# Kernel optimization log

Measured on AMD Instinct MI355X. Metric: run time of the kernel, lower is better.

## Reference

```python
import jax, jax.numpy as jnp
import numpy as np

NUM_HEADS = 16
KEY_SIZE = 128
D_MODEL = NUM_HEADS * KEY_SIZE  # 2048; model_size defaults to num_heads*key_size
B, S = 4, 4096
EPS = 1e-6
MASK_NEG = -1e9


def setup_inputs() -> dict:
    key = jax.random.key(0)
    ks = jax.random.split(key, 8)
    query = jax.random.normal(ks[0], (B, S, D_MODEL), dtype=jnp.float32)
    key_t = jax.random.normal(ks[1], (B, S, D_MODEL), dtype=jnp.float32)
    value = jax.random.normal(ks[2], (B, S, D_MODEL), dtype=jnp.float32)
    # mask broadcast-added to attn_logits of shape [B, S, H, H]; 1 = masked out
    mask = jax.random.randint(ks[3], (B, S, NUM_HEADS, NUM_HEADS), 0, 2).astype(jnp.float32)
    w_scale = 0.02
    Wq = jax.random.normal(ks[4], (D_MODEL, NUM_HEADS * KEY_SIZE), dtype=jnp.float32) * w_scale
    Wk = jax.random.normal(ks[5], (D_MODEL, NUM_HEADS * KEY_SIZE), dtype=jnp.float32) * w_scale
    Wv = jax.random.normal(ks[6], (D_MODEL, NUM_HEADS * KEY_SIZE), dtype=jnp.float32) * w_scale
    Wo = jax.random.normal(ks[7], (NUM_HEADS * KEY_SIZE, D_MODEL), dtype=jnp.float32) * w_scale
    return {"query": query, "key": key_t, "value": value, "mask": mask,
            "Wq": Wq, "Wk": Wk, "Wv": Wv, "Wo": Wo}


def _split_heads(x):
    # [B, S, H*D] -> [B, H, S, D]  (matches tf reshape + transpose(0,2,1,3))
    b, s, _ = x.shape
    return x.reshape(b, s, NUM_HEADS, KEY_SIZE).transpose(0, 2, 1, 3)


def reference(query, key, value, mask, Wq, Wk, Wv, Wo):
    qh = _split_heads(query @ Wq)   # [B, H, S, D]
    kh = _split_heads(key @ Wk)     # [B, H, S, D]
    vh = _split_heads(value @ Wv)   # [B, H, S, D]

    # sum_normalization=True
    qh = qh / (jnp.sum(qh, axis=-1, keepdims=True) + EPS)
    kh = kh / (jnp.sum(kh, axis=-1, keepdims=True) + EPS)

    # Literal tf einsum '...thd,...Thd->...htT' on [B,H,S,D] tensors:
    # t/T bind to the head axis, h binds to the sequence axis.
    # attn_logits: [B, S, H, H]
    attn_logits = jnp.einsum('bqsd,bksd->bsqk', qh, kh)
    attn_logits = attn_logits + mask * MASK_NEG

    # use_softmax=True
    attn_weights = jax.nn.softmax(attn_logits / np.sqrt(float(KEY_SIZE)), axis=-1)

    # Literal tf einsum '...htT,...Thd->...thd' -> [B, H, S, D]
    attn = jnp.einsum('bsqk,bksd->bqsd', attn_weights, vh)
    # _combine_heads: transpose(0,2,1,3) then reshape -> [B, S, H*D]
    attn = attn.transpose(0, 2, 1, 3).reshape(attn.shape[0], attn.shape[2], NUM_HEADS * KEY_SIZE)
    out = attn @ Wo
    return (out, attn_weights)
```

## Files before the change

### kernel.cpp

```cpp
#include <hip/hip_runtime.h>
#include <hip/hip_fp16.h>

#define NHEAD 16
#define DHEAD 128
#define DMODEL 2048
#define SEQ 4096
#define BATCH 4
#define MROWS (BATCH*SEQ)

typedef _Float16 f16x8 __attribute__((ext_vector_type(8)));
typedef _Float16 f16x4 __attribute__((ext_vector_type(4)));
typedef float f32x4 __attribute__((ext_vector_type(4)));

__device__ inline void split8(const float* __restrict__ x, _Float16* __restrict__ hi,
                              _Float16* __restrict__ lo, int i8) {
  float4 v0 = ((const float4*)x)[2 * i8];
  float4 v1 = ((const float4*)x)[2 * i8 + 1];
  f16x8 h, l;
  h[0] = (_Float16)v0.x; h[1] = (_Float16)v0.y;
  h[2] = (_Float16)v0.z; h[3] = (_Float16)v0.w;
  h[4] = (_Float16)v1.x; h[5] = (_Float16)v1.y;
  h[6] = (_Float16)v1.z; h[7] = (_Float16)v1.w;
  ((f16x8*)hi)[i8] = h;
  if (lo) {
    l[0] = (_Float16)(v0.x - (float)h[0]);
    l[1] = (_Float16)(v0.y - (float)h[1]);
    l[2] = (_Float16)(v0.z - (float)h[2]);
    l[3] = (_Float16)(v0.w - (float)h[3]);
    l[4] = (_Float16)(v1.x - (float)h[4]);
    l[5] = (_Float16)(v1.y - (float)h[5]);
    l[6] = (_Float16)(v1.z - (float)h[6]);
    l[7] = (_Float16)(v1.w - (float)h[7]);
    ((f16x8*)lo)[i8] = l;
  }
}

__global__ __launch_bounds__(256) void split_f32_f16(
    const float* __restrict__ x, _Float16* __restrict__ hi,
    _Float16* __restrict__ lo, int n8) {
  int i = blockIdx.x * blockDim.x + threadIdx.x;
  int stride = gridDim.x * blockDim.x;
  for (; i < n8; i += stride) split8(x, hi, lo, i);
}

__device__ inline void transpose_body(const float* __restrict__ W,
                                      _Float16* __restrict__ hi,
                                      _Float16* __restrict__ lo,
                                      int bx, int by, int tx, int ty) {
  __shared__ float tile[32][33];
  int c = bx * 32 + tx;
  for (int r0 = 0; r0 < 32; r0 += 8) {
    int r = by * 32 + ty + r0;
    tile[ty + r0][tx] = W[(size_t)r * DMODEL + c];
  }
  __syncthreads();
  for (int r0 = 0; r0 < 32; r0 += 8) {
    int n = bx * 32 + ty + r0;
    int k = by * 32 + tx;
    float v = tile[tx][ty + r0];
    _Float16 h = (_Float16)v;
    hi[(size_t)n * DMODEL + k] = h;
    if (lo) lo[(size_t)n * DMODEL + k] = (_Float16)(v - (float)h);
  }
}

__global__ __launch_bounds__(256) void transpose_split(
    const float* __restrict__ W, _Float16* __restrict__ hi,
    _Float16* __restrict__ lo) {
  transpose_body(W, hi, lo, blockIdx.x, blockIdx.y, threadIdx.x, threadIdx.y);
}

__device__ inline void colsum_body(const float* __restrict__ W,
                                   float* __restrict__ CS, int k, int t) {
  const int h = t >> 4, s = t & 15;
  double acc = 0.0;
  const float* p = W + (size_t)k * DMODEL + h * DHEAD + s * 8;
#pragma unroll
  for (int i = 0; i < 8; i++) acc += (double)p[i];
#pragma unroll
  for (int m = 1; m < 16; m <<= 1) acc += __shfl_xor(acc, m, 64);
  if (s == 0) CS[(size_t)h * DMODEL + k] = (float)acc;
}

__global__ __launch_bounds__(256) void colsum_f64(
    const float* __restrict__ W, float* __restrict__ CS) {
  colsum_body(W, CS, blockIdx.x, threadIdx.x);
}

__global__ __launch_bounds__(256) void weights_prep(
    const float* __restrict__ Wq, const float* __restrict__ Wk,
    const float* __restrict__ Wv, const float* __restrict__ Wo,
    _Float16* __restrict__ qh, _Float16* __restrict__ ql,
    _Float16* __restrict__ kh, _Float16* __restrict__ kl,
    _Float16* __restrict__ vh, _Float16* __restrict__ oh,
    float* __restrict__ CSq, float* __restrict__ CSk) {
  const int z = blockIdx.z;
  const int t = threadIdx.y * 32 + threadIdx.x;
  if (z == 4) {
    int id = blockIdx.y * 64 + blockIdx.x;
    const float* W = (id & 2048) ? Wk : Wq;
    float* CS = (id & 2048) ? CSk : CSq;
    colsum_body(W, CS, id & 2047, t);
    return;
  }
  const float* W; _Float16* hi; _Float16* lo;
  switch (z) {
    case 0:  W = Wq; hi = qh; lo = ql;      break;
    case 1:  W = Wk; hi = kh; lo = kl;      break;
    case 2:  W = Wv; hi = vh; lo = nullptr; break;
    default: W = Wo; hi = oh; lo = nullptr; break;
  }
  transpose_body(W, hi, lo, blockIdx.x, blockIdx.y, threadIdx.x, threadIdx.y);
}

__global__ __launch_bounds__(256) void prep_qkv(
    const float* __restrict__ q, const float* __restrict__ k,
    const float* __restrict__ v,
    const float* __restrict__ CSq, const float* __restrict__ CSk,
    _Float16* __restrict__ qh, _Float16* __restrict__ ql,
    _Float16* __restrict__ kh, _Float16* __restrict__ kl,
    _Float16* __restrict__ vh,
    float* __restrict__ rsQ, float* __restrict__ rsK) {
  const float* X; const float* CS; float* rs;
  _Float16* hi; _Float16* lo;
  if (blockIdx.y == 0)      { X = q; CS = CSq; rs = rsQ; hi = qh; lo = ql; }
  else if (blockIdx.y == 1) { X = k; CS = CSk; rs = rsK; hi = kh; lo = kl; }
  else                      { X = v; CS = nullptr; rs = nullptr; hi = vh; lo = nullptr; }
  const int t = threadIdx.x;
  const int lane = t & 63, w = t >> 6;
  const int row0 = blockIdx.x * 8 + w * 2;

  const float4* x0 = (const float4*)(X + ((size_t)row0 << 11));
  const float4* x1 = (const float4*)(X + ((size_t)(row0 + 1) << 11));
  float4 xa[8], xb[8];
#pragma unroll
  for (int i = 0; i < 8; i++) {
    xa[i] = x0[i * 64 + lane];
    xb[i] = x1[i * 64 + lane];
  }

  f16x4* hi4 = (f16x4*)hi;
  f16x4* lo4 = (f16x4*)lo;
  const size_t rb0 = (size_t)row0 << 9;
  const size_t rb1 = (size_t)(row0 + 1) << 9;
#pragma unroll
  for (int i = 0; i < 8; i++) {
    int c = i * 64 + lane;
    float4 a = xa[i], b = xb[i];
    f16x4 ha, hb;
    ha[0] = (_Float16)a.x; ha[1] = (_Float16)a.y;
    ha[2] = (_Float16)a.z; ha[3] = (_Float16)a.w;
    hb[0] = (_Float16)b.x; hb[1] = (_Float16)b.y;
    hb[2] = (_Float16)b.z; hb[3] = (_Float16)b.w;
    hi4[rb0 + c] = ha;
    hi4[rb1 + c] = hb;
    if (lo) {
      f16x4 la, lb;
      la[0] = (_Float16)(a.x - (float)ha[0]);
      la[1] = (_Float16)(a.y - (float)ha[1]);
      la[2] = (_Float16)(a.z - (float)ha[2]);
      la[3] = (_Float16)(a.w - (float)ha[3]);
      lb[0] = (_Float16)(b.x - (float)hb[0]);
      lb[1] = (_Float16)(b.y - (float)hb[1]);
      lb[2] = (_Float16)(b.z - (float)hb[2]);
      lb[3] = (_Float16)(b.w - (float)hb[3]);
      lo4[rb0 + c] = la;
      lo4[rb1 + c] = lb;
    }
  }

  if (CS) {
    const float4* cs4 = (const float4*)CS;
    for (int h = 0; h < 16; h++) {
      double a0 = 0.0, a1 = 0.0;
#pragma unroll
      for (int i = 0; i < 8; i++) {
        float4 cv = cs4[h * 512 + i * 64 + lane];
        a0 += (double)xa[i].x * (double)cv.x + (double)xa[i].y * (double)cv.y
            + (double)xa[i].z * (double)cv.z + (double)xa[i].w * (double)cv.w;
        a1 += (double)xb[i].x * (double)cv.x + (double)xb[i].y * (double)cv.y
            + (double)xb[i].z * (double)cv.z + (double)xb[i].w * (double)cv.w;
      }
#pragma unroll
      for (int m = 1; m < 64; m <<= 1) {
        a0 += __shfl_xor(a0, m, 64);
        a1 += __shfl_xor(a1, m, 64);
      }
      if (lane == 0) {
        rs[(size_t)row0 * NHEAD + h]       = (float)a0;
        rs[(size_t)(row0 + 1) * NHEAD + h] = (float)a1;
      }
    }
  }
}

__global__ __launch_bounds__(256) void rowsum_v3(
    const float* __restrict__ q, const float* __restrict__ k,
    const float* __restrict__ CSq, const float* __restrict__ CSk,
    float* __restrict__ rsQ, float* __restrict__ rsK) {
  const float* X;  const float* CS;  float* rs;
  if (blockIdx.y == 0) { X = q; CS = CSq; rs = rsQ; }
  else                 { X = k; CS = CSk; rs = rsK; }
  const int t = threadIdx.x;
  const int lane = t & 63, w = t >> 6;
  const int row0 = blockIdx.x * 8 + w * 2;

  const float4* x0 = (const float4*)(X + ((size_t)row0 << 11));
  const float4* x1 = (const float4*)(X + ((size_t)(row0 + 1) << 11));
  float4 xa[8], xb[8];
#pragma unroll
  for (int i = 0; i < 8; i++) {
    xa[i] = x0[i * 64 + lane];
    xb[i] = x1[i * 64 + lane];
  }
  const float4* cs4 = (const float4*)CS;

  for (int h = 0; h < 16; h++) {
    double a0 = 0.0, a1 = 0.0;
#pragma unroll
    for (int i = 0; i < 8; i++) {
      float4 cv = cs4[h * 512 + i * 64 + lane];
      a0 += (double)xa[i].x * (double)cv.x + (double)xa[i].y * (double)cv.y
          + (double)xa[i].z * (double)cv.z + (double)xa[i].w * (double)cv.w;
      a1 += (double)xb[i].x * (double)cv.x + (double)xb[i].y * (double)cv.y
          + (double)xb[i].z * (double)cv.z + (double)xb[i].w * (double)cv.w;
    }
#pragma unroll
    for (int m = 1; m < 64; m <<= 1) {
      a0 += __shfl_xor(a0, m, 64);
      a1 += __shfl_xor(a1, m, 64);
    }
    if (lane == 0) {
      rs[(size_t)row0 * NHEAD + h]       = (float)a0;
      rs[(size_t)(row0 + 1) * NHEAD + h] = (float)a1;
    }
  }
}

__device__ inline void glds16(const void* g, void* l) {
  __builtin_amdgcn_global_load_lds(
      (const __attribute__((address_space(1))) unsigned int*)g,
      (__attribute__((address_space(3))) unsigned int*)l, 16, 0, 0);
}

#define DP_LGKM_P() do { \
  if constexpr (NPASS == 3) asm volatile("s_waitcnt lgkmcnt(4)" ::: "memory"); \
  else                      asm volatile("s_waitcnt lgkmcnt(2)" ::: "memory"); \
  __builtin_amdgcn_sched_barrier(0); } while (0)
#define DP_LGKM_0() do { \
  asm volatile("s_waitcnt lgkmcnt(0)" ::: "memory"); \
  __builtin_amdgcn_sched_barrier(0); } while (0)
#define DP_VMCNT_P() do { \
  if constexpr (NPASS == 3) asm volatile("s_waitcnt vmcnt(8)" ::: "memory"); \
  else                      asm volatile("s_waitcnt vmcnt(4)" ::: "memory"); \
  __builtin_amdgcn_sched_barrier(0); } while (0)
#define DP_VMCNT_0() do { \
  asm volatile("s_waitcnt vmcnt(0)" ::: "memory"); \
  __builtin_amdgcn_sched_barrier(0); } while (0)
#define DP_BAR() do { \
  asm volatile("" ::: "memory"); \
  __builtin_amdgcn_s_barrier(); \
  asm volatile("" ::: "memory"); } while (0)
#define DP_QUAD(AR, P) do { \
  __builtin_amdgcn_s_setprio(1); \
  _Pragma("unroll") \
  for (int i_ = 0; i_ < 2; i_++) \
    _Pragma("unroll") \
    for (int n_ = 0; n_ < 4; n_++) { \
      acc[2*(P)+i_][n_] = __builtin_amdgcn_mfma_f32_16x16x32_f16(AR[i_], bhF[n_], acc[2*(P)+i_][n_], 0, 0, 0); \
      if constexpr (NPASS == 3) { \
        acc[2*(P)+i_][n_] = __builtin_amdgcn_mfma_f32_16x16x32_f16(AR[i_], blF[n_], acc[2*(P)+i_][n_], 0, 0, 0); \
        acc[2*(P)+i_][n_] = __builtin_amdgcn_mfma_f32_16x16x32_f16(AR[2+i_], bhF[n_], acc[2*(P)+i_][n_], 0, 0, 0); \
      } \
    } \
  __builtin_amdgcn_s_setprio(0); } while (0)

template <int NPASS, int OUT_HALF>
__device__ __forceinline__ void gemm_body(
    int bid, char* smem_raw,
    const _Float16* __restrict__ Ahi, const _Float16* __restrict__ Alo,
    const _Float16* __restrict__ Bhi, const _Float16* __restrict__ Blo,
    float* __restrict__ Cf, _Float16* __restrict__ Ch,
    int M, int N, int Kd) {
  constexpr int NMAT = (NPASS == 3) ? 4 : 2;
  constexpr int NLD  = NMAT * 2;
  constexpr int BUFB = NMAT * 16384;
  constexpr int BOFF = (NPASS == 3) ? 32768 : 16384;

  const int t = threadIdx.x;
  const int lane = t & 63, wid = t >> 6;
  const int wm = wid >> 2, wn = wid & 3;
  const int lr = lane & 15;
  const int lkbs = (((lane >> 4) ^ ((lr >> 1) & 3)) << 4);

  const int mtiles = M >> 8, ntiles = N >> 8;
  const int nwg = mtiles * ntiles;
  const int qq = nwg >> 3;
  const int v = (bid & 7) * qq + (bid >> 3);
  const int m0 = (v / ntiles) << 8, n0 = (v % ntiles) << 8;
  const int NT = Kd >> 5;

  f32x4 acc[8][4] = {};
  f16x8 bhF[4], blF[4], aA[4], aB[4];

  const char* gsrc[NLD];
  int ldst[NLD];
#pragma unroll
  for (int j = 0; j < NLD; j++) {
    int s = t + j * 512;
    int mm = s >> 10;
    int r = (s & 1023) >> 2;
    int g = s & 3;
    int gs = g ^ ((r >> 1) & 3);
    const _Float16* src; int rb;
    if (mm == 0)      { src = Ahi; rb = m0 + r; }
    else if (mm == 1) { src = (NPASS == 3) ? Alo : Bhi;
                        rb = ((NPASS == 3) ? m0 : n0) + r; }
    else if (mm == 2) { src = Bhi; rb = n0 + r; }
    else              { src = Blo; rb = n0 + r; }
    gsrc[j] = (const char*)(src + (size_t)rb * Kd + gs * 8);
    ldst[j] = s * 16;
  }

  auto STAGE = [&](int kt, int c) {
    char* dstb = smem_raw + c * BUFB;
    const size_t kb = (size_t)kt << 6;
#pragma unroll
    for (int j = 0; j < NLD; j++)
      glds16(gsrc[j] + kb, dstb + ldst[j]);
  };
  auto RD_B = [&](const char* buf) {
#pragma unroll
    for (int n = 0; n < 4; n++) {
      int row = wn * 64 + n * 16 + lr;
      bhF[n] = *(const f16x8*)(buf + BOFF + row * 64 + lkbs);
      if constexpr (NPASS == 3)
        blF[n] = *(const f16x8*)(buf + BOFF + 16384 + row * 64 + lkbs);
    }
  };
  auto RD_A = [&](const char* buf, int p, f16x8* d) {
#pragma unroll
    for (int i = 0; i < 2; i++) {
      int row = wm * 128 + (2 * p + i) * 16 + lr;
      d[i] = *(const f16x8*)(buf + row * 64 + lkbs);
      if constexpr (NPASS == 3)
        d[2 + i] = *(const f16x8*)(buf + 16384 + row * 64 + lkbs);
    }
  };

  STAGE(0, 0);
  STAGE(1, 1);
  DP_VMCNT_P();
  DP_BAR();

  for (int kt = 0; kt < NT; kt++) {
    const char* buf = (const char*)smem_raw + (kt & 1) * BUFB;
    RD_B(buf);
    RD_A(buf, 0, aA);
    RD_A(buf, 1, aB);
    DP_LGKM_P();
    DP_QUAD(aA, 0);
    RD_A(buf, 2, aA);
    DP_LGKM_P();
    DP_QUAD(aB, 1);
    RD_A(buf, 3, aB);
    DP_LGKM_P();
    DP_QUAD(aA, 2);
    DP_LGKM_0();
    DP_BAR();
    if (kt + 2 < NT) {
      STAGE(kt + 2, kt & 1);
      DP_QUAD(aB, 3);
      DP_VMCNT_P();
    } else {
      DP_QUAD(aB, 3);
      DP_VMCNT_0();
    }
    DP_BAR();
  }

#pragma unroll
  for (int mi = 0; mi < 8; mi++) {
    int row = m0 + wm * 128 + mi * 16 + ((lane >> 4) << 2);
#pragma unroll
    for (int n = 0; n < 4; n++) {
      int col = n0 + wn * 64 + n * 16 + (lane & 15);
#pragma unroll
      for (int r = 0; r < 4; r++) {
        if constexpr (OUT_HALF)
          Ch[(size_t)(row + r) * N + col] = (_Float16)acc[mi][n][r];
        else
          Cf[(size_t)(row + r) * N + col] = acc[mi][n][r];
      }
    }
  }
}
#undef DP_LGKM_P
#undef DP_LGKM_0
#undef DP_VMCNT_P
#undef DP_VMCNT_0
#undef DP_BAR
#undef DP_QUAD

template <int NPASS, int OUT_HALF>
__global__ __launch_bounds__(512, 1) void gemm_dp(
    const _Float16* __restrict__ Ahi, const _Float16* __restrict__ Alo,
    const _Float16* __restrict__ Bhi, const _Float16* __restrict__ Blo,
    float* __restrict__ Cf, _Float16* __restrict__ Ch,
    int M, int N, int Kd) {
  extern __shared__ char smem_raw[];
  gemm_body<NPASS, OUT_HALF>(blockIdx.x, smem_raw, Ahi, Alo, Bhi, Blo,
                             Cf, Ch, M, N, Kd);
}

__global__ __launch_bounds__(512, 1) void gemm_qkv(
    const _Float16* __restrict__ qh, const _Float16* __restrict__ ql,
    const _Float16* __restrict__ kh, const _Float16* __restrict__ kl,
    const _Float16* __restrict__ vh,
    const _Float16* __restrict__ wqh, const _Float16* __restrict__ wql,
    const _Float16* __restrict__ wkh, const _Float16* __restrict__ wkl,
    const _Float16* __restrict__ wvh,
    float* __restrict__ Qbuf, float* __restrict__ Kbuf,
    _Float16* __restrict__ Vbuf) {
  extern __shared__ char smem_raw[];
  const int bx = blockIdx.x;
  if (bx < 512)
    gemm_body<3, 0>(bx, smem_raw, qh, ql, wqh, wql, Qbuf, nullptr,
                    MROWS, DMODEL, DMODEL);
  else if (bx < 1024)
    gemm_body<3, 0>(bx - 512, smem_raw, kh, kl, wkh, wkl, Kbuf, nullptr,
                    MROWS, DMODEL, DMODEL);
  else
    gemm_body<1, 1>(bx - 1024, smem_raw, vh, nullptr, wvh, nullptr,
                    nullptr, Vbuf, MROWS, DMODEL, DMODEL);
}

template <int NPASS, int OUT_HALF>
__global__ __launch_bounds__(256) void gemm_f16(
    const _Float16* __restrict__ Ahi, const _Float16* __restrict__ Alo,
    const _Float16* __restrict__ Bhi, const _Float16* __restrict__ Blo,
    float* __restrict__ Cf, _Float16* __restrict__ Ch,
    int M, int N, int Kd) {
  constexpr int TILE = 128 * 32;
  __shared__ _Float16 lds[(NPASS == 3 ? 4 : 2) * TILE];
  _Float16* sAh = lds;
  _Float16* sBh = lds + (NPASS == 3 ? 2 : 1) * TILE;
  _Float16* sAl = lds + TILE;
  _Float16* sBl = lds + 3 * TILE;

  const int t = threadIdx.x;
  const int lane = t & 63, wid = t >> 6;
  const int wm = wid >> 1, wn = wid & 1;
  const int lr = lane & 15, lk = (lane >> 4) * 8;

  const int mtiles = M >> 7, ntiles = N >> 7;
  const int nwg = mtiles * ntiles;
  const int qq = nwg >> 3;
  const int v = (blockIdx.x & 7) * qq + (blockIdx.x >> 3);
  const int mx = v / ntiles, ny = v % ntiles;
  const int m0 = mx * 128, n0 = ny * 128;

  f32x4 acc[4][4] = {};

  for (int k0 = 0; k0 < Kd; k0 += 32) {
#pragma unroll
    for (int i = 0; i < 2; i++) {
      int slot = t + i * 256;
      int row = slot >> 2, kc = (slot & 3) * 8;
      glds16(Ahi + (size_t)(m0 + row) * Kd + k0 + kc, sAh + slot * 8);
      glds16(Bhi + (size_t)(n0 + row) * Kd + k0 + kc, sBh + slot * 8);
      if (NPASS == 3) {
        glds16(Alo + (size_t)(m0 + row) * Kd + k0 + kc, sAl + slot * 8);
        glds16(Blo + (size_t)(n0 + row) * Kd + k0 + kc, sBl + slot * 8);
      }
    }
    __syncthreads();

    f16x8 ah[4], bh[4], al[4], bl[4];
#pragma unroll
    for (int f = 0; f < 4; f++) {
      ah[f] = *(const f16x8*)&sAh[(wm * 64 + f * 16 + lr) * 32 + lk];
      bh[f] = *(const f16x8*)&sBh[(wn * 64 + f * 16 + lr) * 32 + lk];
      if (NPASS == 3) {
        al[f] = *(const f16x8*)&sAl[(wm * 64 + f * 16 + lr) * 32 + lk];
        bl[f] = *(const f16x8*)&sBl[(wn * 64 + f * 16 + lr) * 32 + lk];
      }
    }
#pragma unroll
    for (int i = 0; i < 4; i++)
#pragma unroll
      for (int j = 0; j < 4; j++) {
        acc[i][j] = __builtin_amdgcn_mfma_f32_16x16x32_f16(ah[i], bh[j], acc[i][j], 0, 0, 0);
        if (NPASS == 3) {
          acc[i][j] = __builtin_amdgcn_mfma_f32_16x16x32_f16(ah[i], bl[j], acc[i][j], 0, 0, 0);
          acc[i][j] = __builtin_amdgcn_mfma_f32_16x16x32_f16(al[i], bh[j], acc[i][j], 0, 0, 0);
        }
      }
    __syncthreads();
  }

#pragma unroll
  for (int i = 0; i < 4; i++) {
    int row = m0 + wm * 64 + i * 16 + (lane >> 4) * 4;
#pragma unroll
    for (int j = 0; j < 4; j++) {
      int col = n0 + wn * 64 + j * 16 + (lane & 15);
#pragma unroll
      for (int r = 0; r < 4; r++) {
        if (OUT_HALF)
          Ch[(size_t)(row + r) * N + col] = (_Float16)acc[i][j][r];
        else
          Cf[(size_t)(row + r) * N + col] = acc[i][j][r];
      }
    }
  }
}

__global__ __launch_bounds__(256) void attn_kernel(
    const float* __restrict__ Q, const float* __restrict__ K,
    const _Float16* __restrict__ V, const float* __restrict__ mask,
    const float* __restrict__ rsQ, const float* __restrict__ rsK,
    float* __restrict__ wout, _Float16* __restrict__ aout) {
  __shared__ float lq[16][132], lkk[16][132], lv[16][132];
  __shared__ float lw[16][17];
  const int pos = blockIdx.x;
  const int t = threadIdx.x;
  const int h = t >> 4, j = t & 15;
  const size_t rowbase = (size_t)pos * DMODEL + h * DHEAD;

  const float iq = 1.f / (rsQ[(size_t)pos * NHEAD + h] + 1e-6f);
  const float ik = 1.f / (rsK[(size_t)pos * NHEAD + h] + 1e-6f);

  {
    const int dlo = 4 * j, dhi = 64 + 4 * j;
    float4 q0 = *(const float4*)&Q[rowbase + dlo];
    float4 q1 = *(const float4*)&Q[rowbase + dhi];
    q0.x *= iq; q0.y *= iq; q0.z *= iq; q0.w *= iq;
    q1.x *= iq; q1.y *= iq; q1.z *= iq; q1.w *= iq;
    *(float4*)&lq[h][dlo] = q0;
    *(float4*)&lq[h][dhi] = q1;
    float4 k0 = *(const float4*)&K[rowbase + dlo];
    float4 k1 = *(const float4*)&K[rowbase + dhi];
    k0.x *= ik; k0.y *= ik; k0.z *= ik; k0.w *= ik;
    k1.x *= ik; k1.y *= ik; k1.z *= ik; k1.w *= ik;
    *(float4*)&lkk[h][dlo] = k0;
    *(float4*)&lkk[h][dhi] = k1;
    f16x4 v0 = *(const f16x4*)&V[rowbase + dlo];
    f16x4 v1 = *(const f16x4*)&V[rowbase + dhi];
    float4 vf0 = {(float)v0[0], (float)v0[1], (float)v0[2], (float)v0[3]};
    float4 vf1 = {(float)v1[0], (float)v1[1], (float)v1[2], (float)v1[3]};
    *(float4*)&lv[h][dlo] = vf0;
    *(float4*)&lv[h][dhi] = vf1;
  }
  __syncthreads();

  const float4* qr = (const float4*)&lq[h][0];
  const float4* kr = (const float4*)&lkk[j][0];
  float dot = 0.f;
#pragma unroll
  for (int d4 = 0; d4 < 32; d4++) {
    float4 a = qr[d4], b = kr[d4];
    dot = fmaf(a.x, b.x, dot); dot = fmaf(a.y, b.y, dot);
    dot = fmaf(a.z, b.z, dot); dot = fmaf(a.w, b.w, dot);
  }
  float mk = mask[(size_t)pos * 256 + t];
  float x = (dot - 1e9f * mk) * 0.08838834764831845f;
  float mx = x;
#pragma unroll
  for (int m = 1; m < 16; m <<= 1) mx = fmaxf(mx, __shfl_xor(mx, m, 64));
  float e = expf(x - mx);
  float den = e;
#pragma unroll
  for (int m = 1; m < 16; m <<= 1) den += __shfl_xor(den, m, 64);
  float w = e / den;
  wout[(size_t)pos * 256 + t] = w;
  lw[h][j] = w;
  __syncthreads();

  float wreg[16];
#pragma unroll
  for (int k2 = 0; k2 < 16; k2++) wreg[k2] = lw[h][k2];
  float4 a0 = {0.f, 0.f, 0.f, 0.f}, a1 = {0.f, 0.f, 0.f, 0.f};
  const int dlo = 4 * j, dhi = 64 + 4 * j;
#pragma unroll
  for (int k2 = 0; k2 < 16; k2++) {
    float4 v0 = *(const float4*)&lv[k2][dlo];
    float4 v1 = *(const float4*)&lv[k2][dhi];
    float wk = wreg[k2];
    a0.x = fmaf(wk, v0.x, a0.x); a0.y = fmaf(wk, v0.y, a0.y);
    a0.z = fmaf(wk, v0.z, a0.z); a0.w = fmaf(wk, v0.w, a0.w);
    a1.x = fmaf(wk, v1.x, a1.x); a1.y = fmaf(wk, v1.y, a1.y);
    a1.z = fmaf(wk, v1.z, a1.z); a1.w = fmaf(wk, v1.w, a1.w);
  }
  f16x4 o0, o1;
  o0[0] = (_Float16)a0.x; o0[1] = (_Float16)a0.y;
  o0[2] = (_Float16)a0.z; o0[3] = (_Float16)a0.w;
  o1[0] = (_Float16)a1.x; o1[1] = (_Float16)a1.y;
  o1[2] = (_Float16)a1.z; o1[3] = (_Float16)a1.w;
  *(f16x4*)&aout[rowbase + dlo] = o0;
  *(f16x4*)&aout[rowbase + dhi] = o1;
}

extern "C" void kernel_launch(void* const* d_in, const int* in_sizes, int n_in,
                              void* d_out, int out_size, void* d_ws, size_t ws_size,
                              hipStream_t stream) {
  const float* query = (const float*)d_in[0];
  const float* key   = (const float*)d_in[1];
  const float* value = (const float*)d_in[2];
  const float* mask  = (const float*)d_in[3];
  const float* Wq = (const float*)d_in[4];
  const float* Wk = (const float*)d_in[5];
  const float* Wv = (const float*)d_in[6];
  const float* Wo = (const float*)d_in[7];

  float* out  = (float*)d_out;
  float* wout = out + (size_t)MROWS * DMODEL;

  const size_t SZ_HALF = (size_t)MROWS * DMODEL * 2;
  const size_t SZ_F32  = (size_t)MROWS * DMODEL * 4;
  const size_t SZ_W    = (size_t)DMODEL * DMODEL * 2;
  const size_t SZ_CS   = (size_t)DMODEL * NHEAD * 4;
  const size_t SZ_RS   = (size_t)MROWS * NHEAD * 4;

  const int n8 = MROWS * DMODEL / 8;
  const int ggrid = (MROWS / 128) * (DMODEL / 128);
  dim3 wgrid(DMODEL / 32, DMODEL / 32, 5);
  dim3 tgrid(DMODEL / 32, DMODEL / 32);
  dim3 tblk(32, 8);
  dim3 prepgrid(MROWS / 8, 3);
  dim3 rsgrid(MROWS / 8, 2);
  const int dpgrid = (MROWS / 256) * (DMODEL / 256);
  float* Qbuf = out;

  const size_t NEED_A = 5 * SZ_HALF + SZ_F32 + 6 * SZ_W + 2 * SZ_CS + 2 * SZ_RS;
  const size_t NEED_B = 3 * SZ_HALF + SZ_F32 + 2 * SZ_W + 2 * SZ_CS + 2 * SZ_RS;
  char* ws = (char*)d_ws;

  if (ws_size >= NEED_A) {
    size_t off = 0;
    _Float16* qh = (_Float16*)(ws + off); off += SZ_HALF;
    _Float16* ql = (_Float16*)(ws + off); off += SZ_HALF;
    _Float16* kh = (_Float16*)(ws + off); off += SZ_HALF;
    _Float16* kl = (_Float16*)(ws + off); off += SZ_HALF;
    _Float16* vh = (_Float16*)(ws + off); off += SZ_HALF;
    float*  Kbuf = (float*)   (ws + off); off += SZ_F32;
    _Float16* wqh = (_Float16*)(ws + off); off += SZ_W;
    _Float16* wql = (_Float16*)(ws + off); off += SZ_W;
    _Float16* wkh = (_Float16*)(ws + off); off += SZ_W;
    _Float16* wkl = (_Float16*)(ws + off); off += SZ_W;
    _Float16* wvh = (_Float16*)(ws + off); off += SZ_W;
    _Float16* woh = (_Float16*)(ws + off); off += SZ_W;
    float* CSq = (float*)(ws + off); off += SZ_CS;
    float* CSk = (float*)(ws + off); off += SZ_CS;
    float* rsQ = (float*)(ws + off); off += SZ_RS;
    float* rsK = (float*)(ws + off); off += SZ_RS;
    _Float16* Vbuf   = qh;
    _Float16* attn16 = ql;

    weights_prep<<<wgrid, tblk, 0, stream>>>(Wq, Wk, Wv, Wo,
                                             wqh, wql, wkh, wkl, wvh, woh,
                                             CSq, CSk);
    prep_qkv<<<prepgrid, 256, 0, stream>>>(query, key, value, CSq, CSk,
                                           qh, ql, kh, kl, vh, rsQ, rsK);
    gemm_qkv<<<1536, 512, 131072, stream>>>(qh, ql, kh, kl, vh,
                                            wqh, wql, wkh, wkl, wvh,
                                            Qbuf, Kbuf, Vbuf);
    attn_kernel<<<MROWS, 256, 0, stream>>>(Qbuf, Kbuf, Vbuf, mask, rsQ, rsK, wout, attn16);
    gemm_dp<1, 0><<<dpgrid, 512, 65536, stream>>>(attn16, nullptr, woh, nullptr, out, nullptr, MROWS, DMODEL, DMODEL);
    return;
  }

  if (ws_size < NEED_B) return;

  _Float16* a_hi  = (_Float16*)ws;
  _Float16* a_lo  = (_Float16*)(ws + SZ_HALF);
  float*    Kbuf  = (float*)   (ws + 2 * SZ_HALF);
  _Float16* Vbuf  = (_Float16*)(ws + 2 * SZ_HALF + SZ_F32);
  _Float16* wT_hi = (_Float16*)(ws + 3 * SZ_HALF + SZ_F32);
  _Float16* wT_lo = (_Float16*)(ws + 3 * SZ_HALF + SZ_F32 + SZ_W);
  float*    CSq   = (float*)   (ws + 3 * SZ_HALF + SZ_F32 + 2 * SZ_W);
  float*    CSk   = (float*)   (ws + 3 * SZ_HALF + SZ_F32 + 2 * SZ_W + SZ_CS);
  float*    rsQ   = (float*)   (ws + 3 * SZ_HALF + SZ_F32 + 2 * SZ_W + 2 * SZ_CS);
  float*    rsK   = (float*)   (ws + 3 * SZ_HALF + SZ_F32 + 2 * SZ_W + 2 * SZ_CS + SZ_RS);
  _Float16* attn16 = a_hi;

  colsum_f64<<<DMODEL, 256, 0, stream>>>(Wq, CSq);
  colsum_f64<<<DMODEL, 256, 0, stream>>>(Wk, CSk);
  rowsum_v3<<<rsgrid, 256, 0, stream>>>(query, key, CSq, CSk, rsQ, rsK);

  split_f32_f16<<<4096, 256, 0, stream>>>(query, a_hi, a_lo, n8);
  transpose_split<<<tgrid, tblk, 0, stream>>>(Wq, wT_hi, wT_lo);
  gemm_f16<3, 0><<<ggrid, 256, 0, stream>>>(a_hi, a_lo, wT_hi, wT_lo, Qbuf, nullptr, MROWS, DMODEL, DMODEL);
  split_f32_f16<<<4096, 256, 0, stream>>>(key, a_hi, a_lo, n8);
  transpose_split<<<tgrid, tblk, 0, stream>>>(Wk, wT_hi, wT_lo);
  gemm_f16<3, 0><<<ggrid, 256, 0, stream>>>(a_hi, a_lo, wT_hi, wT_lo, Kbuf, nullptr, MROWS, DMODEL, DMODEL);
  split_f32_f16<<<4096, 256, 0, stream>>>(value, a_hi, nullptr, n8);
  transpose_split<<<tgrid, tblk, 0, stream>>>(Wv, wT_hi, nullptr);
  gemm_f16<1, 1><<<ggrid, 256, 0, stream>>>(a_hi, nullptr, wT_hi, nullptr, nullptr, Vbuf, MROWS, DMODEL, DMODEL);
  attn_kernel<<<MROWS, 256, 0, stream>>>(Qbuf, Kbuf, Vbuf, mask, rsQ, rsK, wout, attn16);
  transpose_split<<<tgrid, tblk, 0, stream>>>(Wo, wT_hi, nullptr);
  gemm_f16<1, 0><<<ggrid, 256, 0, stream>>>(attn16, nullptr, wT_hi, nullptr, out, nullptr, MROWS, DMODEL, DMODEL);
}
```

Measured before the change: 1.436 ms.

## Use 128x128 tiled 256-thread GEMM body for fused QKV projection

Replaces the QKV projection GEMM, which used 512-thread workgroups over large tiles with 128KB LDS, by a new 128x128-tile, 256-thread body. It double-buffers 64KB of LDS and allows two workgroups per CU. The grid grows from 1536 to 6144 blocks, and the tile index is swizzled across groups of 8. The aim is better occupancy and load balance and overlap of global loads with MFMA, at the cost of less data reuse per tile and more global traffic.

```diff
diff --git a/kernel.cpp b/kernel.cpp
--- a/kernel.cpp
+++ b/kernel.cpp
@@ -413,7 +413,157 @@
                              Cf, Ch, M, N, Kd);
 }
 
-__global__ __launch_bounds__(512, 1) void gemm_qkv(
+#define D8_LGKM(n3, n1) do { \
+  if constexpr (NPASS == 3) asm volatile("s_waitcnt lgkmcnt(" #n3 ")" ::: "memory"); \
+  else                      asm volatile("s_waitcnt lgkmcnt(" #n1 ")" ::: "memory"); \
+  __builtin_amdgcn_sched_barrier(0); } while (0)
+#define D8_VMCNT_P() do { \
+  if constexpr (NPASS == 3) asm volatile("s_waitcnt vmcnt(8)" ::: "memory"); \
+  else                      asm volatile("s_waitcnt vmcnt(4)" ::: "memory"); \
+  __builtin_amdgcn_sched_barrier(0); } while (0)
+#define D8_VMCNT_0() do { \
+  asm volatile("s_waitcnt vmcnt(0)" ::: "memory"); \
+  __builtin_amdgcn_sched_barrier(0); } while (0)
+#define D8_BAR() do { \
+  asm volatile("" ::: "memory"); \
+  __builtin_amdgcn_s_barrier(); \
+  asm volatile("" ::: "memory"); } while (0)
+#define D8_QUAD(AR, P) do { \
+  __builtin_amdgcn_s_setprio(1); \
+  _Pragma("unroll") \
+  for (int n_ = 0; n_ < 4; n_++) { \
+    acc[P][n_] = __builtin_amdgcn_mfma_f32_16x16x32_f16(AR[0], bhF[n_], acc[P][n_], 0, 0, 0); \
+    if constexpr (NPASS == 3) { \
+      acc[P][n_] = __builtin_amdgcn_mfma_f32_16x16x32_f16(AR[0], blF[n_], acc[P][n_], 0, 0, 0); \
+      acc[P][n_] = __builtin_amdgcn_mfma_f32_16x16x32_f16(AR[1], bhF[n_], acc[P][n_], 0, 0, 0); \
+    } \
+  } \
+  __builtin_amdgcn_s_setprio(0); } while (0)
+
+template <int NPASS, int OUT_HALF>
+__device__ __forceinline__ void gemm_body128(
+    int bid, char* smem_raw,
+    const _Float16* __restrict__ Ahi, const _Float16* __restrict__ Alo,
+    const _Float16* __restrict__ Bhi, const _Float16* __restrict__ Blo,
+    float* __restrict__ Cf, _Float16* __restrict__ Ch,
+    int M, int N, int Kd) {
+  constexpr int NMAT = (NPASS == 3) ? 4 : 2;
+  constexpr int NLD  = NMAT * 2;
+  constexpr int BUFB = NMAT * 8192;
+  constexpr int BOFF = (NPASS == 3) ? 16384 : 8192;
+
+  const int t = threadIdx.x;
+  const int lane = t & 63, wid = t >> 6;
+  const int wm = wid >> 1, wn = wid & 1;
+  const int lr = lane & 15;
+  const int lkbs = (((lane >> 4) ^ ((lr >> 1) & 3)) << 4);
+
+  const int mtiles = M >> 7, ntiles = N >> 7;
+  const int nwg = mtiles * ntiles;
+  const int qq = nwg >> 3;
+  const int v = (bid & 7) * qq + (bid >> 3);
+  const int m0 = (v / ntiles) << 7, n0 = (v % ntiles) << 7;
+  const int NT = Kd >> 5;
+
+  f32x4 acc[4][4] = {};
+  f16x8 bhF[4], blF[4], aA[2], aB[2];
+
+  const char* gsrc[NLD];
+  int ldst[NLD];
+#pragma unroll
+  for (int j = 0; j < NLD; j++) {
+    int s = t + j * 256;
+    int mm = s >> 9;
+    int r = (s & 511) >> 2;
+    int g = s & 3;
+    int gs = g ^ ((r >> 1) & 3);
+    const _Float16* src; int rb;
+    if (mm == 0)      { src = Ahi; rb = m0 + r; }
+    else if (mm == 1) { src = (NPASS == 3) ? Alo : Bhi;
+                        rb = ((NPASS == 3) ? m0 : n0) + r; }
+    else if (mm == 2) { src = Bhi; rb = n0 + r; }
+    else              { src = Blo; rb = n0 + r; }
+    gsrc[j] = (const char*)(src + (size_t)rb * Kd + gs * 8);
+    ldst[j] = s * 16;
+  }
+
+  auto STAGE = [&](int kt, int c) {
+    char* dstb = smem_raw + c * BUFB;
+    const size_t kb = (size_t)kt << 6;
+#pragma unroll
+    for (int j = 0; j < NLD; j++)
+      glds16(gsrc[j] + kb, dstb + ldst[j]);
+  };
+  auto RD_B = [&](const char* buf) {
+#pragma unroll
+    for (int n = 0; n < 4; n++) {
+      int row = wn * 64 + n * 16 + lr;
+      bhF[n] = *(const f16x8*)(buf + BOFF + row * 64 + lkbs);
+      if constexpr (NPASS == 3)
+        blF[n] = *(const f16x8*)(buf + BOFF + 8192 + row * 64 + lkbs);
+    }
+  };
+  auto RD_A = [&](const char* buf, int p, f16x8* d) {
+    int row = wm * 64 + p * 16 + lr;
+    d[0] = *(const f16x8*)(buf + row * 64 + lkbs);
+    if constexpr (NPASS == 3)
+      d[1] = *(const f16x8*)(buf + 8192 + row * 64 + lkbs);
+  };
+
+  STAGE(0, 0);
+  STAGE(1, 1);
+  D8_VMCNT_P();
+  D8_BAR();
+
+  for (int kt = 0; kt < NT; kt++) {
+    const char* buf = (const char*)smem_raw + (kt & 1) * BUFB;
+    RD_B(buf);
+    RD_A(buf, 0, aA);
+    RD_A(buf, 1, aB);
+    D8_LGKM(2, 1);
+    D8_QUAD(aA, 0);
+    RD_A(buf, 2, aA);
+    D8_LGKM(2, 1);
+    D8_QUAD(aB, 1);
+    RD_A(buf, 3, aB);
+    D8_LGKM(2, 1);
+    D8_QUAD(aA, 2);
+    D8_LGKM(0, 0);
+    D8_BAR();
+    if (kt + 2 < NT) {
+      STAGE(kt + 2, kt & 1);
+      D8_QUAD(aB, 3);
+      D8_VMCNT_P();
+    } else {
+      D8_QUAD(aB, 3);
+      D8_VMCNT_0();
+    }
+    D8_BAR();
+  }
+
+#pragma unroll
+  for (int i = 0; i < 4; i++) {
+    int row = m0 + wm * 64 + i * 16 + ((lane >> 4) << 2);
+#pragma unroll
+    for (int j = 0; j < 4; j++) {
+      int col = n0 + wn * 64 + j * 16 + (lane & 15);
+#pragma unroll
+      for (int r = 0; r < 4; r++) {
+        if constexpr (OUT_HALF)
+          Ch[(size_t)(row + r) * N + col] = (_Float16)acc[i][j][r];
+        else
+          Cf[(size_t)(row + r) * N + col] = acc[i][j][r];
+      }
+    }
+  }
+}
+#undef D8_LGKM
+#undef D8_VMCNT_P
+#undef D8_VMCNT_0
+#undef D8_BAR
+#undef D8_QUAD
+
+__global__ __launch_bounds__(256, 2) void gemm_qkv128(
     const _Float16* __restrict__ qh, const _Float16* __restrict__ ql,
     const _Float16* __restrict__ kh, const _Float16* __restrict__ kl,
     const _Float16* __restrict__ vh,
@@ -424,15 +574,15 @@
     _Float16* __restrict__ Vbuf) {
   extern __shared__ char smem_raw[];
   const int bx = blockIdx.x;
-  if (bx < 512)
-    gemm_body<3, 0>(bx, smem_raw, qh, ql, wqh, wql, Qbuf, nullptr,
-                    MROWS, DMODEL, DMODEL);
-  else if (bx < 1024)
-    gemm_body<3, 0>(bx - 512, smem_raw, kh, kl, wkh, wkl, Kbuf, nullptr,
-                    MROWS, DMODEL, DMODEL);
+  if (bx < 2048)
+    gemm_body128<3, 0>(bx, smem_raw, qh, ql, wqh, wql, Qbuf, nullptr,
+                       MROWS, DMODEL, DMODEL);
+  else if (bx < 4096)
+    gemm_body128<3, 0>(bx - 2048, smem_raw, kh, kl, wkh, wkl, Kbuf, nullptr,
+                       MROWS, DMODEL, DMODEL);
   else
-    gemm_body<1, 1>(bx - 1024, smem_raw, vh, nullptr, wvh, nullptr,
-                    nullptr, Vbuf, MROWS, DMODEL, DMODEL);
+    gemm_body128<1, 1>(bx - 4096, smem_raw, vh, nullptr, wvh, nullptr,
+                       nullptr, Vbuf, MROWS, DMODEL, DMODEL);
 }
 
 template <int NPASS, int OUT_HALF>
@@ -662,9 +812,9 @@
                                              CSq, CSk);
     prep_qkv<<<prepgrid, 256, 0, stream>>>(query, key, value, CSq, CSk,
                                            qh, ql, kh, kl, vh, rsQ, rsK);
-    gemm_qkv<<<1536, 512, 131072, stream>>>(qh, ql, kh, kl, vh,
-                                            wqh, wql, wkh, wkl, wvh,
-                                            Qbuf, Kbuf, Vbuf);
+    gemm_qkv128<<<6144, 256, 65536, stream>>>(qh, ql, kh, kl, vh,
+                                              wqh, wql, wkh, wkl, wvh,
+                                              Qbuf, Kbuf, Vbuf);
     attn_kernel<<<MROWS, 256, 0, stream>>>(Qbuf, Kbuf, Vbuf, mask, rsQ, rsK, wout, attn16);
     gemm_dp<1, 0><<<dpgrid, 512, 65536, stream>>>(attn16, nullptr, woh, nullptr, out, nullptr, MROWS, DMODEL, DMODEL);
     return;
```

After: 1.549 ms. 7.9% more time.
